# Performance work log

Hardware: AMD Instinct MI355X
Metric: run time of the kernel (lower is better)

Reference implementation:

```python
import jax, jax.numpy as jnp
import numpy as np

# Network dimensions (match init_kwargs)
N_IN, N_HID, N_OUT = 2048, 8192, 1024
N = N_IN + N_HID + N_OUT
BATCH = 512


def setup_inputs() -> dict:
    key = jax.random.key(0)
    k_w, k_b, k_x = jax.random.split(key, 3)
    # GraphNet._init_connections: Xavier-ish std based on (n_inputs + n_outputs)
    std = (2.0 / (N_IN + N_OUT)) ** 0.5
    W = jax.random.normal(k_w, (N, N), dtype=jnp.float32) * std
    # mask: inputs -> hidden, hidden -> outputs (fixed 3-level DAG)
    mask = jnp.zeros((N, N), dtype=jnp.float32)
    mask = mask.at[:N_IN, N_IN:N_IN + N_HID].set(1.0)
    mask = mask.at[N_IN:N_IN + N_HID, N_IN + N_HID:].set(1.0)
    # bias is zero-init in the module; use small random values so it is exercised
    bias = jax.random.normal(k_b, (N,), dtype=jnp.float32) * 0.01
    x = jax.random.normal(k_x, (BATCH, N_IN), dtype=jnp.float32)
    return {"x": x, "W": W, "bias": bias, "mask": mask}


def reference(x, W, bias, mask):
    # Faithful translation of GraphNet.forward for the canonical 3-level
    # topology produced by _init_connections/_compute_levels:
    #   level 0: input nodes [0, N_IN)
    #   level 1: hidden nodes [N_IN, N_IN+N_HID)  -> ReLU
    #   level 2: output nodes [N_IN+N_HID, N)     -> identity (OUTPUT type)
    W_eff = W * mask                       # [N, N] masked adjacency
    B = x.shape[0]
    h = jnp.zeros((B, N), dtype=x.dtype).at[:, :N_IN].set(x)
    # level 1 (hidden): pre_act = h @ W_eff[:, idx] + bias[idx]; ReLU
    pre_h = h @ W_eff[:, N_IN:N_IN + N_HID] + bias[N_IN:N_IN + N_HID]
    h = h.at[:, N_IN:N_IN + N_HID].set(jax.nn.relu(pre_h))
    # level 2 (outputs): pre-activation only (node_type == OUTPUT -> no ReLU)
    pre_o = h @ W_eff[:, N_IN + N_HID:] + bias[N_IN + N_HID:]
    return pre_o                            # h[:, output_indices]
```

## Files before the change

kernel.cpp:

```cpp
#include <hip/hip_runtime.h>

#define N_IN 2048
#define N_HID 8192
#define N_OUT 1024
#define NTOT 11264

typedef __attribute__((ext_vector_type(4))) float f32x4;
typedef __attribute__((ext_vector_type(4))) short short4v;
typedef __attribute__((ext_vector_type(8))) short short8v;
typedef __attribute__((ext_vector_type(2))) unsigned u32x2;

__device__ inline short f2bf(float f) {
    unsigned u = __float_as_uint(f);
    return (short)((u + 0x7fffu + ((u >> 16) & 1u)) >> 16);
}

__device__ inline float bf2f(short s) {
    return __uint_as_float(((unsigned)(unsigned short)s) << 16);
}

__device__ inline unsigned cvt_pk_bf16(float lo, float hi) {
    unsigned r;
    asm("v_cvt_pk_bf16_f32 %0, %1, %2" : "=v"(r) : "v"(lo), "v"(hi));
    return r;
}

__device__ inline int perm64(int c) {
    return (c & 32) + (((c >> 2) & 3) << 3) + (((c >> 4) & 1) << 2) + (c & 3);
}

__device__ inline void gload_lds16(const void* g, void* l) {
    __builtin_amdgcn_global_load_lds(
        (const __attribute__((address_space(1))) unsigned int*)g,
        (__attribute__((address_space(3))) unsigned int*)l, 16, 0, 0);
}

__global__ __launch_bounds__(256) void cvt_x(
    const float* __restrict__ x, short* __restrict__ xb)
{
    const int i = blockIdx.x * 256 + threadIdx.x;
    const f32x4 v = *reinterpret_cast<const f32x4*>(x + (size_t)i * 4);
    u32x2 s;
    s[0] = cvt_pk_bf16(v[0], v[1]);
    s[1] = cvt_pk_bf16(v[2], v[3]);
    const int c0  = (i * 4) & (N_IN - 1);
    const int p   = (c0 & ~63) + perm64(c0 & 63);
    const size_t row = (size_t)(i >> 9);
    *reinterpret_cast<u32x2*>(xb + row * N_IN + p) = s;
}

template<bool FUSE>
__global__ __launch_bounds__(512, 2) void gemm_bf16(
    const short* __restrict__ A,
    const float* __restrict__ W,
    const float* __restrict__ bias,
    short* __restrict__ hOut,
    short* __restrict__ pOut,
    int lda, int nt, int wrow0, int wcol0)
{
    __shared__ __align__(16) short As[4][128 * 64];
    __shared__ __align__(16) short Bs[2][128][72];

    const int t    = threadIdx.x;
    const int lane = t & 63;
    const int wid  = t >> 6;
    const int wr   = wid >> 2;
    const int wc   = wid & 3;
    const int brow = blockIdx.y * 128;
    const int bcol = blockIdx.x * 128;
    const int l15  = lane & 15;
    const int lg   = lane >> 4;
    const int ks   = blockIdx.z * 1024;

    const int arow = lane >> 3;
    const int asw  = ((lane & 7) * 16) ^ (arow << 4);

    const int nb   = (lane & 7) + 8 * (wid >> 1);
    const int kblk = ((lane >> 3) & 7) + 8 * (wid & 1);
    const int n0 = nb * 4, k0 = kblk * 4;
    const int p0 = perm64(k0);

    const char*  Abytes = (const char*)A;
    const size_t lda_b  = (size_t)lda * 2;

    f32x4 acc[4][2] = {};
    f32x4 bv0[4], bv1[4], bv2[4], bv3[4];

    const float* wp0 = &W[(size_t)(wrow0 + ks + k0) * NTOT + (wcol0 + bcol + n0)];

#define B_LOAD(TT, BV) { \
    const float* wp = wp0 + (size_t)(TT) * 64 * NTOT; \
    _Pragma("unroll") for (int j = 0; j < 4; ++j) \
        BV[j] = *reinterpret_cast<const f32x4*>(wp + (size_t)j * NTOT); }

#define A_LOAD(TT) { \
    char* dst = (char*)As + ((TT) & 3) * 16384; \
    _Pragma("unroll") for (int i = 0; i < 2; ++i) { \
        const int c = wid * 2 + i; \
        gload_lds16(Abytes + (size_t)(brow + c * 8 + arow) * lda_b \
                          + (size_t)(ks + (TT) * 64) * 2 + asw, \
                    dst + c * 1024); } }

#define B_WRITE(TT, BV) { \
    short* bsb = &Bs[(TT) & 1][0][0]; \
    _Pragma("unroll") for (int i = 0; i < 4; ++i) { \
        u32x2 s; \
        s[0] = cvt_pk_bf16(BV[0][i], BV[1][i]); \
        s[1] = cvt_pk_bf16(BV[2][i], BV[3][i]); \
        *reinterpret_cast<u32x2*>(bsb + (n0 + i) * 72 + p0) = s; } }

#define COMPUTE(TT) { \
    const char*  ab = (const char*)As + ((TT) & 3) * 16384; \
    const short* bb = &Bs[(TT) & 1][0][0]; \
    short8v a[2][4], b[2][2]; \
    _Pragma("unroll") for (int g = 0; g < 2; ++g) { \
        const int koff = g * 64 + lg * 16; \
        _Pragma("unroll") for (int m = 0; m < 4; ++m) { \
            const int r = wr * 64 + m * 16 + l15; \
            a[g][m] = *reinterpret_cast<const short8v*>( \
                ab + ((r * 128 + koff) ^ ((r & 7) << 4))); } \
        _Pragma("unroll") for (int n = 0; n < 2; ++n) { \
            const int r = wc * 32 + n * 16 + l15; \
            b[g][n] = *reinterpret_cast<const short8v*>( \
                (const char*)(bb + r * 72) + koff); } } \
    __builtin_amdgcn_s_setprio(1); \
    _Pragma("unroll") for (int g = 0; g < 2; ++g) \
      _Pragma("unroll") for (int m = 0; m < 4; ++m) \
        _Pragma("unroll") for (int n = 0; n < 2; ++n) \
            acc[m][n] = __builtin_amdgcn_mfma_f32_16x16x32_bf16( \
                a[g][m], b[g][n], acc[m][n], 0, 0, 0); \
    __builtin_amdgcn_s_setprio(0); }

#define WAITV(N) { asm volatile("s_waitcnt vmcnt(" #N ")" ::: "memory"); \
                   __builtin_amdgcn_sched_barrier(0); }
#define BARRIER  { asm volatile("s_waitcnt lgkmcnt(0)" ::: "memory"); \
                   __builtin_amdgcn_sched_barrier(0); \
                   __builtin_amdgcn_s_barrier(); \
                   __builtin_amdgcn_sched_barrier(0); }

#define ITER(T, BVL, BVW) { \
    B_LOAD(T + 3, BVL); A_LOAD(T + 3); \
    WAITV(12); \
    B_WRITE(T + 1, BVW); \
    COMPUTE(T); \
    BARRIER; }

    B_LOAD(0, bv0); A_LOAD(0);
    B_LOAD(1, bv1); A_LOAD(1);
    B_LOAD(2, bv2); A_LOAD(2);
    WAITV(12);
    B_WRITE(0, bv0);
    BARRIER;

    for (int tt = 0; tt + 4 < nt; tt += 4) {
        ITER(tt,     bv3, bv1);
        ITER(tt + 1, bv0, bv2);
        ITER(tt + 2, bv1, bv3);
        ITER(tt + 3, bv2, bv0);
    }
    ITER(nt - 4, bv3, bv1);

    WAITV(6);
    B_WRITE(nt - 2, bv2);
    COMPUTE(nt - 3);
    BARRIER;
    WAITV(0);
    B_WRITE(nt - 1, bv3);
    COMPUTE(nt - 2);
    BARRIER;
    COMPUTE(nt - 1);

#undef B_LOAD
#undef A_LOAD
#undef B_WRITE
#undef COMPUTE
#undef WAITV
#undef BARRIER
#undef ITER

    if (FUSE) {
#pragma unroll
        for (int m = 0; m < 4; ++m) {
            const int row0 = brow + wr * 64 + m * 16 + lg * 4;
#pragma unroll
            for (int n = 0; n < 2; ++n) {
                const int col  = bcol + wc * 32 + n * 16 + l15;
                const int pcol = (col & ~63) + perm64(col & 63);
                const float bb = bias[N_IN + col];
#pragma unroll
                for (int q = 0; q < 4; ++q) {
                    float v = acc[m][n][q] + bb;
                    v = v > 0.f ? v : 0.f;
                    hOut[(size_t)(row0 + q) * N_HID + pcol] = f2bf(v);
                }
            }
        }
    } else {
        short* po = pOut + (size_t)blockIdx.z * (512 * N_OUT);
#pragma unroll
        for (int m = 0; m < 4; ++m) {
            const int row0 = brow + wr * 64 + m * 16 + lg * 4;
#pragma unroll
            for (int n = 0; n < 2; ++n) {
                const int col = bcol + wc * 32 + n * 16 + l15;
#pragma unroll
                for (int q = 0; q < 4; ++q)
                    po[(size_t)(row0 + q) * N_OUT + col] = f2bf(acc[m][n][q]);
            }
        }
    }
}

__global__ __launch_bounds__(256) void reduce_bias(
    const short* __restrict__ part,
    const float* __restrict__ bias,
    float* __restrict__ out)
{
    const int idx = (blockIdx.x * 256 + threadIdx.x) * 4;
    f32x4 s = *reinterpret_cast<const f32x4*>(&bias[N_IN + N_HID + (idx & 1023)]);
#pragma unroll
    for (int sp = 0; sp < 8; ++sp) {
        const short4v p = *reinterpret_cast<const short4v*>(
            &part[(size_t)sp * 524288 + idx]);
#pragma unroll
        for (int j = 0; j < 4; ++j) s[j] += bf2f(p[j]);
    }
    *reinterpret_cast<f32x4*>(&out[idx]) = s;
}

extern "C" void kernel_launch(void* const* d_in, const int* in_sizes, int n_in,
                              void* d_out, int out_size, void* d_ws, size_t ws_size,
                              hipStream_t stream) {
    const float* x    = (const float*)d_in[0];
    const float* W    = (const float*)d_in[1];
    const float* bias = (const float*)d_in[2];
    float* out = (float*)d_out;

    short* h    = (short*)d_ws;
    short* part = (short*)((char*)d_ws + (size_t)(8 << 20));
    short* xb   = (short*)((char*)d_ws + (size_t)(8 << 20));

    cvt_x<<<dim3(1024), dim3(256), 0, stream>>>(x, xb);

    gemm_bf16<true><<<dim3(64, 4, 1), dim3(512), 0, stream>>>(
        xb, W, bias, h, nullptr, N_IN, 32, 0, N_IN);

    gemm_bf16<false><<<dim3(8, 4, 8), dim3(512), 0, stream>>>(
        h, W, nullptr, nullptr, part, N_HID, 16, N_IN, N_IN + N_HID);

    reduce_bias<<<dim3(512), dim3(256), 0, stream>>>(part, bias, out);
}
```

Before: 68.31 us.

## Double K-tile to 128 per stage and rework pipeline to two-deep buffering

Each pipeline stage now covers a K extent of 128 instead of 64. The A and B LDS buffers are reshaped to two slots of two 64-wide halves, and the pipeline drops from four-deep prefetch to two-deep, which halves the number of barriers and loop iterations. In exchange, each thread holds more W registers per stage (two sets of 8 f32x4) and there is less prefetch lookahead to hide global-load latency. The epilogue and the vmcnt waits are rewritten to match the new stage count.

```diff
diff --git a/kernel.cpp b/kernel.cpp
--- a/kernel.cpp
+++ b/kernel.cpp
@@ -58,8 +58,8 @@
     short* __restrict__ pOut,
     int lda, int nt, int wrow0, int wcol0)
 {
-    __shared__ __align__(16) short As[4][128 * 64];
-    __shared__ __align__(16) short Bs[2][128][72];
+    __shared__ __align__(16) short As[2][128 * 128];
+    __shared__ __align__(16) short Bs[2][2 * 128 * 72];
 
     const int t    = threadIdx.x;
     const int lane = t & 63;
@@ -83,53 +83,64 @@
     const char*  Abytes = (const char*)A;
     const size_t lda_b  = (size_t)lda * 2;
 
+    const char* aG0 = Abytes + (size_t)(brow + (wid * 2 + 0) * 8 + arow) * lda_b
+                             + (size_t)ks * 2 + asw;
+    const char* aG1 = Abytes + (size_t)(brow + (wid * 2 + 1) * 8 + arow) * lda_b
+                             + (size_t)ks * 2 + asw;
+    const int ldsAoff = wid * 2048;
+
     f32x4 acc[4][2] = {};
-    f32x4 bv0[4], bv1[4], bv2[4], bv3[4];
+    f32x4 bvE[8], bvO[8];
 
     const float* wp0 = &W[(size_t)(wrow0 + ks + k0) * NTOT + (wcol0 + bcol + n0)];
 
 #define B_LOAD(TT, BV) { \
-    const float* wp = wp0 + (size_t)(TT) * 64 * NTOT; \
+    const float* wp = wp0 + (size_t)(TT) * 128 * NTOT; \
     _Pragma("unroll") for (int j = 0; j < 4; ++j) \
-        BV[j] = *reinterpret_cast<const f32x4*>(wp + (size_t)j * NTOT); }
+        BV[j] = *reinterpret_cast<const f32x4*>(wp + (size_t)j * NTOT); \
+    _Pragma("unroll") for (int j = 4; j < 8; ++j) \
+        BV[j] = *reinterpret_cast<const f32x4*>(wp + (size_t)(j + 60) * NTOT); }
 
 #define A_LOAD(TT) { \
-    char* dst = (char*)As + ((TT) & 3) * 16384; \
-    _Pragma("unroll") for (int i = 0; i < 2; ++i) { \
-        const int c = wid * 2 + i; \
-        gload_lds16(Abytes + (size_t)(brow + c * 8 + arow) * lda_b \
-                          + (size_t)(ks + (TT) * 64) * 2 + asw, \
-                    dst + c * 1024); } }
+    char* dst = (char*)As + ((TT) & 1) * 32768; \
+    gload_lds16(aG0 + (size_t)(TT) * 256,       dst + ldsAoff); \
+    gload_lds16(aG1 + (size_t)(TT) * 256,       dst + ldsAoff + 1024); \
+    gload_lds16(aG0 + (size_t)(TT) * 256 + 128, dst + 16384 + ldsAoff); \
+    gload_lds16(aG1 + (size_t)(TT) * 256 + 128, dst + 16384 + ldsAoff + 1024); }
 
 #define B_WRITE(TT, BV) { \
-    short* bsb = &Bs[(TT) & 1][0][0]; \
+    char* bsb = (char*)Bs + ((TT) & 1) * 36864; \
     _Pragma("unroll") for (int i = 0; i < 4; ++i) { \
-        u32x2 s; \
-        s[0] = cvt_pk_bf16(BV[0][i], BV[1][i]); \
-        s[1] = cvt_pk_bf16(BV[2][i], BV[3][i]); \
-        *reinterpret_cast<u32x2*>(bsb + (n0 + i) * 72 + p0) = s; } }
+        u32x2 s0, s1; \
+        s0[0] = cvt_pk_bf16(BV[0][i], BV[1][i]); \
+        s0[1] = cvt_pk_bf16(BV[2][i], BV[3][i]); \
+        s1[0] = cvt_pk_bf16(BV[4][i], BV[5][i]); \
+        s1[1] = cvt_pk_bf16(BV[6][i], BV[7][i]); \
+        *reinterpret_cast<u32x2*>(bsb + (n0 + i) * 144 + p0 * 2) = s0; \
+        *reinterpret_cast<u32x2*>(bsb + 18432 + (n0 + i) * 144 + p0 * 2) = s1; } }
 
 #define COMPUTE(TT) { \
-    const char*  ab = (const char*)As + ((TT) & 3) * 16384; \
-    const short* bb = &Bs[(TT) & 1][0][0]; \
-    short8v a[2][4], b[2][2]; \
-    _Pragma("unroll") for (int g = 0; g < 2; ++g) { \
-        const int koff = g * 64 + lg * 16; \
-        _Pragma("unroll") for (int m = 0; m < 4; ++m) { \
-            const int r = wr * 64 + m * 16 + l15; \
-            a[g][m] = *reinterpret_cast<const short8v*>( \
-                ab + ((r * 128 + koff) ^ ((r & 7) << 4))); } \
-        _Pragma("unroll") for (int n = 0; n < 2; ++n) { \
-            const int r = wc * 32 + n * 16 + l15; \
-            b[g][n] = *reinterpret_cast<const short8v*>( \
-                (const char*)(bb + r * 72) + koff); } } \
-    __builtin_amdgcn_s_setprio(1); \
-    _Pragma("unroll") for (int g = 0; g < 2; ++g) \
-      _Pragma("unroll") for (int m = 0; m < 4; ++m) \
-        _Pragma("unroll") for (int n = 0; n < 2; ++n) \
-            acc[m][n] = __builtin_amdgcn_mfma_f32_16x16x32_bf16( \
-                a[g][m], b[g][n], acc[m][n], 0, 0, 0); \
-    __builtin_amdgcn_s_setprio(0); }
+    _Pragma("unroll") for (int g2 = 0; g2 < 2; ++g2) { \
+        const char* ab = (const char*)As + ((TT) & 1) * 32768 + g2 * 16384; \
+        const char* bb = (const char*)Bs + ((TT) & 1) * 36864 + g2 * 18432; \
+        short8v a[2][4], b[2][2]; \
+        _Pragma("unroll") for (int g = 0; g < 2; ++g) { \
+            const int koff = g * 64 + lg * 16; \
+            _Pragma("unroll") for (int m = 0; m < 4; ++m) { \
+                const int r = wr * 64 + m * 16 + l15; \
+                a[g][m] = *reinterpret_cast<const short8v*>( \
+                    ab + ((r * 128 + koff) ^ ((r & 7) << 4))); } \
+            _Pragma("unroll") for (int n = 0; n < 2; ++n) { \
+                const int r = wc * 32 + n * 16 + l15; \
+                b[g][n] = *reinterpret_cast<const short8v*>( \
+                    bb + r * 144 + koff); } } \
+        __builtin_amdgcn_s_setprio(1); \
+        _Pragma("unroll") for (int g = 0; g < 2; ++g) \
+          _Pragma("unroll") for (int m = 0; m < 4; ++m) \
+            _Pragma("unroll") for (int n = 0; n < 2; ++n) \
+                acc[m][n] = __builtin_amdgcn_mfma_f32_16x16x32_bf16( \
+                    a[g][m], b[g][n], acc[m][n], 0, 0, 0); \
+        __builtin_amdgcn_s_setprio(0); } }
 
 #define WAITV(N) { asm volatile("s_waitcnt vmcnt(" #N ")" ::: "memory"); \
                    __builtin_amdgcn_sched_barrier(0); }
@@ -139,34 +150,31 @@
                    __builtin_amdgcn_sched_barrier(0); }
 
 #define ITER(T, BVL, BVW) { \
-    B_LOAD(T + 3, BVL); A_LOAD(T + 3); \
-    WAITV(12); \
+    A_LOAD(T + 1); \
+    B_LOAD(T + 2, BVL); \
+    WAITV(12);               \
     B_WRITE(T + 1, BVW); \
     COMPUTE(T); \
+    WAITV(8);                \
     BARRIER; }
 
-    B_LOAD(0, bv0); A_LOAD(0);
-    B_LOAD(1, bv1); A_LOAD(1);
-    B_LOAD(2, bv2); A_LOAD(2);
-    WAITV(12);
-    B_WRITE(0, bv0);
+    B_LOAD(0, bvE);
+    A_LOAD(0);
+    B_LOAD(1, bvO);
+    WAITV(8);
+    B_WRITE(0, bvE);
     BARRIER;
 
-    for (int tt = 0; tt + 4 < nt; tt += 4) {
-        ITER(tt,     bv3, bv1);
-        ITER(tt + 1, bv0, bv2);
-        ITER(tt + 2, bv1, bv3);
-        ITER(tt + 3, bv2, bv0);
+    for (int tt = 0; tt + 3 < nt; tt += 2) {
+        ITER(tt,     bvE, bvO);
+        ITER(tt + 1, bvO, bvE);
     }
-    ITER(nt - 4, bv3, bv1);
-
-    WAITV(6);
-    B_WRITE(nt - 2, bv2);
-    COMPUTE(nt - 3);
-    BARRIER;
+
+    A_LOAD(nt - 1);
+    WAITV(4);
+    B_WRITE(nt - 1, bvO);
+    COMPUTE(nt - 2);
     WAITV(0);
-    B_WRITE(nt - 1, bv3);
-    COMPUTE(nt - 2);
     BARRIER;
     COMPUTE(nt - 1);
 
@@ -243,10 +251,10 @@
     cvt_x<<<dim3(1024), dim3(256), 0, stream>>>(x, xb);
 
     gemm_bf16<true><<<dim3(64, 4, 1), dim3(512), 0, stream>>>(
-        xb, W, bias, h, nullptr, N_IN, 32, 0, N_IN);
+        xb, W, bias, h, nullptr, N_IN, 16, 0, N_IN);
 
     gemm_bf16<false><<<dim3(8, 4, 8), dim3(512), 0, stream>>>(
-        h, W, nullptr, nullptr, part, N_HID, 16, N_IN, N_IN + N_HID);
+        h, W, nullptr, nullptr, part, N_HID, 8, N_IN, N_IN + N_HID);
 
     reduce_bias<<<dim3(512), dim3(256), 0, stream>>>(part, bias, out);
 }
```

Measured after the change: 69.89 us. 2.3% more time.
